# Performance work log

Measured on AMD Instinct MI355X. Metric: run time of the kernel, lower is better.

## Reference

```python
import jax, jax.numpy as jnp
import numpy as np
from jax import lax

# LNS semantics: values are held as (sign, log_base|x|); exact conversion round-trips
# make log-domain mul/add mathematically identical to float conv/linear/relu, so the
# faithful reference is the equivalent float pipeline.

def _conv(x, w, b):
    # x: [B,C,H,W], w: [O,C,kh,kw] (torch layout), stride 1, no padding
    y = lax.conv_general_dilated(x, w, window_strides=(1, 1), padding='VALID',
                                 dimension_numbers=('NCHW', 'OIHW', 'NCHW'))
    return y + b[None, :, None, None]

def _maxpool2(x):
    return lax.reduce_window(x, -jnp.inf, lax.max,
                             window_dimensions=(1, 1, 2, 2),
                             window_strides=(1, 1, 2, 2), padding='VALID')

def setup_inputs() -> dict:
    key = jax.random.key(0)
    ks = jax.random.split(key, 9)
    s = lambda k, shape, fan: jax.random.normal(k, shape, jnp.float32) * (1.0 / np.sqrt(fan))
    return {
        'x': jax.random.normal(ks[0], (512, 1, 54, 54), jnp.float32),
        'conv1_w': s(ks[1], (32, 1, 3, 3), 9),
        'conv1_b': s(ks[2], (32,), 9),
        'conv2_w': s(ks[3], (64, 32, 3, 3), 32 * 9),
        'conv2_b': s(ks[4], (64,), 32 * 9),
        'fc1_w': s(ks[5], (128, 9216), 9216),
        'fc1_b': s(ks[6], (128,), 9216),
        'fc2_w': s(ks[7], (10, 128), 128),
        'fc2_b': s(ks[8], (10,), 128),
    }

def reference(x, conv1_w, conv1_b, conv2_w, conv2_b, fc1_w, fc1_b, fc2_w, fc2_b):
    h = jnp.maximum(_conv(x, conv1_w, conv1_b), 0.0)          # [B,32,52,52]
    h = _maxpool2(h)                                          # [B,32,26,26]
    h = jnp.maximum(_conv(h, conv2_w, conv2_b), 0.0)          # [B,64,24,24]
    h = _maxpool2(h)                                          # [B,64,12,12]
    h = h.reshape(h.shape[0], -1)                             # [B,9216]
    h = jnp.maximum(h @ fc1_w.T + fc1_b, 0.0)                 # [B,128]
    return h @ fc2_w.T + fc2_b                                # [B,10]
```

## Files before the change

kernel.cpp:

```cpp
#include <hip/hip_runtime.h>


#define B 512
#define POS 676
#define ICP 36
#define P2SZ (64*12*12)

typedef unsigned short ushort_t;
typedef ushort_t ushort4v __attribute__((ext_vector_type(4)));
typedef short s16x8 __attribute__((ext_vector_type(8)));
typedef float f32x4 __attribute__((ext_vector_type(4)));

__device__ __forceinline__ ushort_t f2bf(float f) {
    union { float f; unsigned u; } a; a.f = f;
    unsigned r = a.u + 0x7FFFu + ((a.u >> 16) & 1u);
    return (ushort_t)(r >> 16);
}
__device__ __forceinline__ float bf2f(ushort_t u) {
    union { unsigned u; float f; } a; a.u = ((unsigned)u) << 16;
    return a.f;
}

#define N_WR (64 * 9 * 32)
#define N_WF (128 * 9216)
#define CONV1_BLOCKS 1664
#define PREP_BLOCKS  4680

__global__ __launch_bounds__(256) void conv1_prep(const float* __restrict__ x,
                                                  const float* __restrict__ w,
                                                  const float* __restrict__ bias,
                                                  const float* __restrict__ c2w,
                                                  const float* __restrict__ f1w,
                                                  ushort_t* __restrict__ out,
                                                  ushort_t* __restrict__ wr,
                                                  ushort_t* __restrict__ wfb) {
    int blk = blockIdx.x;
    if (blk >= CONV1_BLOCKS) {
        int t = (blk - CONV1_BLOCKS) * 256 + threadIdx.x;
        if (t < N_WR) {
            int ic  = t & 31;
            int tap = (t >> 5) % 9;
            int oc  = t / 288;
            wr[t] = f2bf(c2w[oc * 288 + ic * 9 + tap]);
        } else if (t < N_WR + N_WF) {
            int i = t - N_WR;
            wfb[i] = f2bf(f1w[i]);
        }
        return;
    }
    int t = blk * 256 + threadIdx.x;
    int ic = t & 31;
    int r  = t >> 5;
    int py = r % 26;
    int b  = r / 26;

    const float* wp = w + ic * 9;
    float w00 = wp[0], w01 = wp[1], w02 = wp[2];
    float w10 = wp[3], w11 = wp[4], w12 = wp[5];
    float w20 = wp[6], w21 = wp[7], w22 = wp[8];
    float bv = bias[ic];

    const float* xr = x + b * (54 * 54) + (2 * py) * 54;
    ushort_t* po = out + ((size_t)b * POS + py * 26) * 32 + ic;

    float2 p[4], q[4];
#pragma unroll
    for (int rr = 0; rr < 4; ++rr) p[rr] = *reinterpret_cast<const float2*>(xr + rr * 54);
#pragma unroll
    for (int rr = 0; rr < 4; ++rr) q[rr] = *reinterpret_cast<const float2*>(xr + rr * 54 + 2);

#pragma unroll
    for (int px = 0; px < 26; ++px) {
        float s00 = p[0].x * w00 + p[0].y * w01 + q[0].x * w02
                  + p[1].x * w10 + p[1].y * w11 + q[1].x * w12
                  + p[2].x * w20 + p[2].y * w21 + q[2].x * w22;
        float s01 = p[0].y * w00 + q[0].x * w01 + q[0].y * w02
                  + p[1].y * w10 + q[1].x * w11 + q[1].y * w12
                  + p[2].y * w20 + q[2].x * w21 + q[2].y * w22;
        float s10 = p[1].x * w00 + p[1].y * w01 + q[1].x * w02
                  + p[2].x * w10 + p[2].y * w11 + q[2].x * w12
                  + p[3].x * w20 + p[3].y * w21 + q[3].x * w22;
        float s11 = p[1].y * w00 + q[1].x * w01 + q[1].y * w02
                  + p[2].y * w10 + q[2].x * w11 + q[2].y * w12
                  + p[3].y * w20 + q[3].x * w21 + q[3].y * w22;
        float m = fmaxf(fmaxf(s00, s01), fmaxf(s10, s11));
        po[px * 32] = f2bf(fmaxf(m + bv, 0.0f));
        if (px < 25) {
#pragma unroll
            for (int rr = 0; rr < 4; ++rr) {
                p[rr] = q[rr];
                q[rr] = *reinterpret_cast<const float2*>(xr + rr * 54 + 2 * px + 4);
            }
        }
    }
}

__global__ __launch_bounds__(256) void conv2_mfma(const ushort_t* __restrict__ p1,
                                                  const ushort_t* __restrict__ wr,
                                                  const float* __restrict__ bias,
                                                  ushort_t* __restrict__ pool2) {
    __shared__ ushort_t lds[260 * ICP];
    int blk = blockIdx.x;
    int b = blk / 3, c = blk % 3;
    int tid = threadIdx.x;

    const ushort_t* src = p1 + ((size_t)b * POS + 8 * c * 26) * 32;
    for (int t = tid; t < 260 * 8; t += 256) {
        int pos = t >> 3, off = (t & 7) * 4;
        ushort4v v = *reinterpret_cast<const ushort4v*>(src + pos * 32 + off);
        *reinterpret_cast<ushort4v*>(&lds[pos * ICP + off]) = v;
    }
    __syncthreads();

    int lane = tid & 63, wid = tid >> 6;
    int quad = lane >> 4, lr = lane & 15;

    int ebase[3];
#pragma unroll
    for (int t = 0; t < 3; ++t) {
        int m  = t * 16 + lr;
        int yl = m / 24;
        int xx = m - yl * 24;
        ebase[t] = ((2 * wid + yl) * 26 + xx) * ICP + quad * 8;
    }

    f32x4 acc[3][4];
#pragma unroll
    for (int t = 0; t < 3; ++t)
#pragma unroll
        for (int n = 0; n < 4; ++n) acc[t][n] = (f32x4){0.f, 0.f, 0.f, 0.f};

    const ushort_t* wb = wr + (size_t)lr * 288 + quad * 8;

#pragma unroll
    for (int tap = 0; tap < 9; ++tap) {
        int ky = tap / 3, kx = tap % 3;
        int koff = (ky * 26 + kx) * ICP;
        s16x8 a[3];
#pragma unroll
        for (int t = 0; t < 3; ++t) {
            union { ushort4v s[2]; s16x8 v; } u;
            u.s[0] = *reinterpret_cast<const ushort4v*>(&lds[ebase[t] + koff]);
            u.s[1] = *reinterpret_cast<const ushort4v*>(&lds[ebase[t] + koff + 4]);
            a[t] = u.v;
        }
        s16x8 bf[4];
#pragma unroll
        for (int n = 0; n < 4; ++n)
            bf[n] = *reinterpret_cast<const s16x8*>(wb + n * 4608 + tap * 32);
#pragma unroll
        for (int t = 0; t < 3; ++t)
#pragma unroll
            for (int n = 0; n < 4; ++n)
                acc[t][n] = __builtin_amdgcn_mfma_f32_16x16x32_bf16(a[t], bf[n], acc[t][n], 0, 0, 0);
    }
    __syncthreads();

    ushort_t* scr = lds + wid * 1536;
#pragma unroll
    for (int t = 0; t < 3; ++t)
#pragma unroll
        for (int n = 0; n < 4; ++n) {
            int oc = n * 16 + lr;
            int i0 = t * 8 + quad * 2;
            float v0 = fmaxf(acc[t][n][0], acc[t][n][1]);
            float v1 = fmaxf(acc[t][n][2], acc[t][n][3]);
            union { ushort_t u2[2]; unsigned w; } pk;
            pk.u2[0] = f2bf(v0); pk.u2[1] = f2bf(v1);
            *reinterpret_cast<unsigned*>(&scr[oc * 24 + i0]) = pk.w;
        }
    int oc = lane;
    const ushort_t* row = scr + oc * 24;
    float bv = bias[oc];
    int py = c * 4 + wid;
    ushort_t outv[12];
#pragma unroll
    for (int px = 0; px < 12; ++px) {
        float r0 = bf2f(row[px]);
        float r1 = bf2f(row[px + 12]);
        outv[px] = f2bf(fmaxf(fmaxf(r0, r1) + bv, 0.0f));
    }
    ushort_t* po = pool2 + ((size_t)(b * 64 + oc) * 144 + py * 12);
#pragma unroll
    for (int q = 0; q < 3; ++q)
        *reinterpret_cast<ushort4v*>(po + q * 4) =
            (ushort4v){outv[q*4+0], outv[q*4+1], outv[q*4+2], outv[q*4+3]};
}

__global__ __launch_bounds__(256) void fc1_mfma(const ushort_t* __restrict__ A,
                                                 const ushort_t* __restrict__ W,
                                                 float* __restrict__ Cpart) {
    int tid = threadIdx.x;
    int lane = tid & 63, wid = tid >> 6;
    int lr = lane & 15, quad = lane >> 4;
    int w  = blockIdx.x * 4 + wid;
    int nt = w & 7;
    int ks = (w >> 3) & 15;
    int mt = w >> 7;

    int m  = mt * 16 + lr;
    int k0 = ks * 576;
    const ushort_t* arow = A + (size_t)m * 9216 + k0 + quad * 8;
    const ushort_t* wrow = W + (size_t)(nt * 16 + lr) * 9216 + k0 + quad * 8;

    f32x4 acc = (f32x4){0.f, 0.f, 0.f, 0.f};
#pragma unroll
    for (int kk = 0; kk < 18; ++kk) {
        s16x8 a   = *reinterpret_cast<const s16x8*>(arow + kk * 32);
        s16x8 bfr = *reinterpret_cast<const s16x8*>(wrow + kk * 32);
        acc = __builtin_amdgcn_mfma_f32_16x16x32_bf16(a, bfr, acc, 0, 0, 0);
    }

    float* cp = Cpart + (size_t)ks * (512 * 128);
    int crow = mt * 16 + quad * 4;
#pragma unroll
    for (int r = 0; r < 4; ++r)
        cp[(size_t)(crow + r) * 128 + nt * 16 + lr] = acc[r];
}

__global__ __launch_bounds__(128) void fc1fc2(const float* __restrict__ Cpart,
                                              const float* __restrict__ b1,
                                              const float* __restrict__ w2,
                                              const float* __restrict__ b2,
                                              float* __restrict__ out) {
    __shared__ float h[128];
    int b = blockIdx.x, k = threadIdx.x;
    float s = 0.f;
#pragma unroll
    for (int ks = 0; ks < 16; ++ks) s += Cpart[(size_t)ks * (512 * 128) + b * 128 + k];
    h[k] = fmaxf(s + b1[k], 0.0f);
    __syncthreads();
    if (k < 10) {
        const float* wp = w2 + k * 128;
        float acc = 0.f;
#pragma unroll 8
        for (int j = 0; j < 128; ++j) acc += h[j] * wp[j];
        out[b * 10 + k] = acc + b2[k];
    }
}

extern "C" void kernel_launch(void* const* d_in, const int* in_sizes, int n_in,
                              void* d_out, int out_size, void* d_ws, size_t ws_size,
                              hipStream_t stream) {
    const float* x       = (const float*)d_in[0];
    const float* conv1_w = (const float*)d_in[1];
    const float* conv1_b = (const float*)d_in[2];
    const float* conv2_w = (const float*)d_in[3];
    const float* conv2_b = (const float*)d_in[4];
    const float* fc1_w   = (const float*)d_in[5];
    const float* fc1_b   = (const float*)d_in[6];
    const float* fc2_w   = (const float*)d_in[7];
    const float* fc2_b   = (const float*)d_in[8];
    float* out = (float*)d_out;

    char* ws = (char*)d_ws;
    ushort_t* pool1 = (ushort_t*)ws;
    ws += (size_t)B * POS * 32 * sizeof(ushort_t);
    ushort_t* wr = (ushort_t*)ws;
    ws += N_WR * sizeof(ushort_t) + 128;
    ushort_t* wfb = (ushort_t*)ws;
    ws += N_WF * sizeof(ushort_t) + 128;
    ushort_t* pool2b = (ushort_t*)ws;
    ws += (size_t)B * P2SZ * sizeof(ushort_t) + 128;
    float* Cpart = (float*)ws;
    ws += (size_t)16 * 512 * 128 * sizeof(float) + 128;

    {
        conv1_prep<<<CONV1_BLOCKS + PREP_BLOCKS, 256, 0, stream>>>(
            x, conv1_w, conv1_b, conv2_w, fc1_w, pool1, wr, wfb);
    }
    {
        conv2_mfma<<<B * 3, 256, 0, stream>>>(pool1, wr, conv2_b, pool2b);
    }
    {
        fc1_mfma<<<1024, 256, 0, stream>>>(pool2b, wfb, Cpart);
    }
    {
        fc1fc2<<<B, 128, 0, stream>>>(Cpart, fc1_b, fc2_w, fc2_b, out);
    }
}
```

Measured before the change: 137.6 us.

## Use 2x2 MFMA register tiles in fc1 with finer split-K; pack conv1 math

The fc1 kernel now gives each wave a 32x32 output tile built from four 16x16 MFMAs, so every loaded A and W fragment is reused twice. The K dimension is split into 32 slices instead of 16, and the launch drops to 512 blocks. The point is to cut redundant global loads of activations and weights per MFMA. The cost is twice as large a partial-sum buffer for the reduction kernel to read. Separately, conv1 computes its 2x2 pool window with float2 vector arithmetic so the compiler can emit packed FP32 ops.

```diff
diff --git a/kernel.cpp b/kernel.cpp
--- a/kernel.cpp
+++ b/kernel.cpp
@@ -10,6 +10,7 @@
 typedef ushort_t ushort4v __attribute__((ext_vector_type(4)));
 typedef short s16x8 __attribute__((ext_vector_type(8)));
 typedef float f32x4 __attribute__((ext_vector_type(4)));
+typedef float f32x2 __attribute__((ext_vector_type(2)));
 
 __device__ __forceinline__ ushort_t f2bf(float f) {
     union { float f; unsigned u; } a; a.f = f;
@@ -63,33 +64,32 @@
     const float* xr = x + b * (54 * 54) + (2 * py) * 54;
     ushort_t* po = out + ((size_t)b * POS + py * 26) * 32 + ic;
 
-    float2 p[4], q[4];
-#pragma unroll
-    for (int rr = 0; rr < 4; ++rr) p[rr] = *reinterpret_cast<const float2*>(xr + rr * 54);
-#pragma unroll
-    for (int rr = 0; rr < 4; ++rr) q[rr] = *reinterpret_cast<const float2*>(xr + rr * 54 + 2);
+    f32x2 p[4], q[4];
+#pragma unroll
+    for (int rr = 0; rr < 4; ++rr) p[rr] = *reinterpret_cast<const f32x2*>(xr + rr * 54);
+#pragma unroll
+    for (int rr = 0; rr < 4; ++rr) q[rr] = *reinterpret_cast<const f32x2*>(xr + rr * 54 + 2);
 
 #pragma unroll
     for (int px = 0; px < 26; ++px) {
-        float s00 = p[0].x * w00 + p[0].y * w01 + q[0].x * w02
-                  + p[1].x * w10 + p[1].y * w11 + q[1].x * w12
-                  + p[2].x * w20 + p[2].y * w21 + q[2].x * w22;
-        float s01 = p[0].y * w00 + q[0].x * w01 + q[0].y * w02
-                  + p[1].y * w10 + q[1].x * w11 + q[1].y * w12
-                  + p[2].y * w20 + q[2].x * w21 + q[2].y * w22;
-        float s10 = p[1].x * w00 + p[1].y * w01 + q[1].x * w02
-                  + p[2].x * w10 + p[2].y * w11 + q[2].x * w12
-                  + p[3].x * w20 + p[3].y * w21 + q[3].x * w22;
-        float s11 = p[1].y * w00 + q[1].x * w01 + q[1].y * w02
-                  + p[2].y * w10 + q[2].x * w11 + q[2].y * w12
-                  + p[3].y * w20 + q[3].x * w21 + q[3].y * w22;
-        float m = fmaxf(fmaxf(s00, s01), fmaxf(s10, s11));
+        f32x2 mid[4];
+#pragma unroll
+        for (int rr = 0; rr < 4; ++rr) mid[rr] = (f32x2){p[rr].y, q[rr].x};
+
+        f32x2 s0 = p[0] * (f32x2)w00 + mid[0] * (f32x2)w01 + q[0] * (f32x2)w02
+                 + p[1] * (f32x2)w10 + mid[1] * (f32x2)w11 + q[1] * (f32x2)w12
+                 + p[2] * (f32x2)w20 + mid[2] * (f32x2)w21 + q[2] * (f32x2)w22;
+        f32x2 s1 = p[1] * (f32x2)w00 + mid[1] * (f32x2)w01 + q[1] * (f32x2)w02
+                 + p[2] * (f32x2)w10 + mid[2] * (f32x2)w11 + q[2] * (f32x2)w12
+                 + p[3] * (f32x2)w20 + mid[3] * (f32x2)w21 + q[3] * (f32x2)w22;
+
+        float m = fmaxf(fmaxf(s0.x, s0.y), fmaxf(s1.x, s1.y));
         po[px * 32] = f2bf(fmaxf(m + bv, 0.0f));
         if (px < 25) {
 #pragma unroll
             for (int rr = 0; rr < 4; ++rr) {
                 p[rr] = q[rr];
-                q[rr] = *reinterpret_cast<const float2*>(xr + rr * 54 + 2 * px + 4);
+                q[rr] = *reinterpret_cast<const f32x2*>(xr + rr * 54 + 2 * px + 4);
             }
         }
     }
@@ -194,28 +194,48 @@
     int lane = tid & 63, wid = tid >> 6;
     int lr = lane & 15, quad = lane >> 4;
     int w  = blockIdx.x * 4 + wid;
-    int nt = w & 7;
-    int ks = (w >> 3) & 15;
+    int nt = w & 3;
+    int ks = (w >> 2) & 31;
     int mt = w >> 7;
 
-    int m  = mt * 16 + lr;
-    int k0 = ks * 576;
-    const ushort_t* arow = A + (size_t)m * 9216 + k0 + quad * 8;
-    const ushort_t* wrow = W + (size_t)(nt * 16 + lr) * 9216 + k0 + quad * 8;
-
-    f32x4 acc = (f32x4){0.f, 0.f, 0.f, 0.f};
-#pragma unroll
-    for (int kk = 0; kk < 18; ++kk) {
-        s16x8 a   = *reinterpret_cast<const s16x8*>(arow + kk * 32);
-        s16x8 bfr = *reinterpret_cast<const s16x8*>(wrow + kk * 32);
-        acc = __builtin_amdgcn_mfma_f32_16x16x32_bf16(a, bfr, acc, 0, 0, 0);
+    int m0 = mt * 32;
+    int n0 = nt * 32;
+    int k0 = ks * 288 + quad * 8;
+    const ushort_t* a0 = A + (size_t)(m0 + lr) * 9216 + k0;
+    const ushort_t* a1 = a0 + (size_t)16 * 9216;
+    const ushort_t* b0 = W + (size_t)(n0 + lr) * 9216 + k0;
+    const ushort_t* b1 = b0 + (size_t)16 * 9216;
+
+    f32x4 acc[2][2];
+#pragma unroll
+    for (int i = 0; i < 2; ++i)
+#pragma unroll
+        for (int j = 0; j < 2; ++j) acc[i][j] = (f32x4){0.f, 0.f, 0.f, 0.f};
+
+#pragma unroll
+    for (int kk = 0; kk < 9; ++kk) {
+        s16x8 av0 = *reinterpret_cast<const s16x8*>(a0 + kk * 32);
+        s16x8 av1 = *reinterpret_cast<const s16x8*>(a1 + kk * 32);
+        s16x8 bv0 = *reinterpret_cast<const s16x8*>(b0 + kk * 32);
+        s16x8 bv1 = *reinterpret_cast<const s16x8*>(b1 + kk * 32);
+        acc[0][0] = __builtin_amdgcn_mfma_f32_16x16x32_bf16(av0, bv0, acc[0][0], 0, 0, 0);
+        acc[0][1] = __builtin_amdgcn_mfma_f32_16x16x32_bf16(av0, bv1, acc[0][1], 0, 0, 0);
+        acc[1][0] = __builtin_amdgcn_mfma_f32_16x16x32_bf16(av1, bv0, acc[1][0], 0, 0, 0);
+        acc[1][1] = __builtin_amdgcn_mfma_f32_16x16x32_bf16(av1, bv1, acc[1][1], 0, 0, 0);
     }
 
     float* cp = Cpart + (size_t)ks * (512 * 128);
-    int crow = mt * 16 + quad * 4;
-#pragma unroll
-    for (int r = 0; r < 4; ++r)
-        cp[(size_t)(crow + r) * 128 + nt * 16 + lr] = acc[r];
+#pragma unroll
+    for (int i = 0; i < 2; ++i) {
+        int crow = m0 + i * 16 + quad * 4;
+#pragma unroll
+        for (int j = 0; j < 2; ++j) {
+            int col = n0 + j * 16 + lr;
+#pragma unroll
+            for (int r = 0; r < 4; ++r)
+                cp[(size_t)(crow + r) * 128 + col] = acc[i][j][r];
+        }
+    }
 }
 
 __global__ __launch_bounds__(128) void fc1fc2(const float* __restrict__ Cpart,
@@ -227,7 +247,7 @@
     int b = blockIdx.x, k = threadIdx.x;
     float s = 0.f;
 #pragma unroll
-    for (int ks = 0; ks < 16; ++ks) s += Cpart[(size_t)ks * (512 * 128) + b * 128 + k];
+    for (int ks = 0; ks < 32; ++ks) s += Cpart[(size_t)ks * (512 * 128) + b * 128 + k];
     h[k] = fmaxf(s + b1[k], 0.0f);
     __syncthreads();
     if (k < 10) {
@@ -263,7 +283,7 @@
     ushort_t* pool2b = (ushort_t*)ws;
     ws += (size_t)B * P2SZ * sizeof(ushort_t) + 128;
     float* Cpart = (float*)ws;
-    ws += (size_t)16 * 512 * 128 * sizeof(float) + 128;
+    ws += (size_t)32 * 512 * 128 * sizeof(float) + 128;
 
     {
         conv1_prep<<<CONV1_BLOCKS + PREP_BLOCKS, 256, 0, stream>>>(
@@ -273,7 +293,7 @@
         conv2_mfma<<<B * 3, 256, 0, stream>>>(pool1, wr, conv2_b, pool2b);
     }
     {
-        fc1_mfma<<<1024, 256, 0, stream>>>(pool2b, wfb, Cpart);
+        fc1_mfma<<<512, 256, 0, stream>>>(pool2b, wfb, Cpart);
     }
     {
         fc1fc2<<<B, 128, 0, stream>>>(Cpart, fc1_b, fc2_w, fc2_b, out);
```

After: 131.3 us. 1.05x faster.
